# Performance work log

Measured on AMD Instinct MI355X. Metric: run time of the kernel, lower is better.

## Reference

```python
import jax, jax.numpy as jnp
import numpy as np

HEIGHT = 256
WIDTH = 256
SIGMAINV = 7000.0  # DIB-R style soft-silhouette sharpness
EPS = 1e-10


def setup_inputs():
    key = jax.random.key(0)
    k1, k2, k3, k4, k5 = jax.random.split(key, 5)
    B, P, F = 1, 160, 256
    TH = TW = 1024
    points_bxpx3 = 0.8 * jax.random.normal(k1, (B, P, 3), jnp.float32)
    faces_fx3 = jax.random.randint(k2, (F, 3), 0, P)
    camera_rot_bx3x3 = jnp.broadcast_to(jnp.eye(3, dtype=jnp.float32), (B, 3, 3))
    camera_pos_bx3 = jnp.tile(jnp.array([[0.0, 0.0, 2.5]], jnp.float32), (B, 1))
    camera_proj_3x1 = jnp.array([[2.5], [2.5], [-1.0]], jnp.float32)
    uv_bxpx2 = jax.random.uniform(k3, (B, P, 2), jnp.float32)
    ft_fx3 = jax.random.randint(k4, (F, 3), 0, P)
    texture_bx3xthxtw = jax.random.uniform(k5, (B, 3, TH, TW), jnp.float32)
    return {"points_bxpx3": points_bxpx3, "faces_fx3": faces_fx3,
            "camera_rot_bx3x3": camera_rot_bx3x3, "camera_pos_bx3": camera_pos_bx3,
            "camera_proj_3x1": camera_proj_3x1, "uv_bxpx2": uv_bxpx2,
            "ft_fx3": ft_fx3, "texture_bx3xthxtw": texture_bx3xthxtw}


def _perspective(points_bxpx3, faces_fx3, cam_rot, cam_pos, cam_proj):
    p = points_bxpx3 - cam_pos[:, None, :]
    p = jnp.einsum('bpj,bij->bpi', p, cam_rot)                  # camera frame [B,P,3]
    xy3 = p * cam_proj.reshape(1, 1, 3)
    xy = xy3[..., :2] / xy3[..., 2:3]                           # projected 2D [B,P,2]
    pf0 = p[:, faces_fx3[:, 0]]
    pf1 = p[:, faces_fx3[:, 1]]
    pf2 = p[:, faces_fx3[:, 2]]
    points3d_bxfx9 = jnp.concatenate([pf0, pf1, pf2], axis=2)
    points2d_bxfx6 = jnp.concatenate([xy[:, faces_fx3[:, 0]], xy[:, faces_fx3[:, 1]], xy[:, faces_fx3[:, 2]]], axis=2)
    normal_bxfx3 = jnp.cross(pf1 - pf0, pf2 - pf0)
    return points3d_bxfx9, points2d_bxfx6, normal_bxfx3


def _edge_dist2(px, py, ax, ay, bx, by):
    ex, ey = bx - ax, by - ay
    t = jnp.clip(((px - ax) * ex + (py - ay) * ey) / (ex * ex + ey * ey + EPS), 0.0, 1.0)
    dx, dy = px - (ax + t * ex), py - (ay + t * ey)
    return dx * dx + dy * dy


def _rasterize(points3d_bxfx9, points2d_bxfx6, normalz_bxfx1, feat_bxfx9, H, W):
    B, F, _ = points2d_bxfx6.shape
    x0, y0, x1, y1, x2, y2 = [points2d_bxfx6[:, None, :, i] for i in range(6)]   # [B,1,F]
    xs = (jnp.arange(W, dtype=jnp.float32) + 0.5) / W * 2.0 - 1.0
    ys = 1.0 - (jnp.arange(H, dtype=jnp.float32) + 0.5) / H * 2.0
    px = jnp.tile(xs[None, :], (H, 1)).reshape(1, -1, 1)                          # [1,N,1]
    py = jnp.tile(ys[:, None], (1, W)).reshape(1, -1, 1)
    A = (x1 - x0) * (y2 - y0) - (x2 - x0) * (y1 - y0)
    invA = jnp.where(jnp.abs(A) > EPS, 1.0 / jnp.where(jnp.abs(A) > EPS, A, 1.0), 0.0)
    w0 = ((x1 - px) * (y2 - py) - (x2 - px) * (y1 - py)) * invA                   # [B,N,F]
    w1 = ((x2 - px) * (y0 - py) - (x0 - px) * (y2 - py)) * invA
    w2 = 1.0 - w0 - w1
    valid = (jnp.abs(A) > EPS) & (normalz_bxfx1[:, None, :, 0] > 0)               # backface cull
    inside = (w0 >= 0) & (w1 >= 0) & (w2 >= 0) & valid
    z0 = points3d_bxfx9[:, None, :, 2]
    z1 = points3d_bxfx9[:, None, :, 5]
    z2 = points3d_bxfx9[:, None, :, 8]
    z = w0 * z0 + w1 * z1 + w2 * z2                                               # camera looks down -z
    fid = jnp.argmax(jnp.where(inside, z, -1e10), axis=2)                          # nearest covering face
    hit = jnp.any(inside, axis=2)
    take = lambda a: jnp.take_along_axis(a, fid[:, :, None], axis=2)[:, :, 0]
    w0s, w1s, w2s = take(w0), take(w1), take(w2)
    fverts = feat_bxfx9.reshape(B, F, 3, 3)
    fsel = jax.vmap(lambda fv, ii: fv[ii])(fverts, fid)                            # [B,N,3verts,3feat]
    imfeat = (w0s[..., None] * fsel[:, :, 0] + w1s[..., None] * fsel[:, :, 1] + w2s[..., None] * fsel[:, :, 2])
    imfeat = imfeat * hit[..., None].astype(imfeat.dtype)
    # soft silhouette probability (DIB-R): 1 - prod_f (1 - exp(-d^2 * sigmainv))
    d2 = jnp.minimum(_edge_dist2(px, py, x0, y0, x1, y1),
                     jnp.minimum(_edge_dist2(px, py, x1, y1, x2, y2),
                                 _edge_dist2(px, py, x2, y2, x0, y0)))
    d2 = jnp.where(inside, 0.0, d2)
    log_miss = jnp.log(jnp.clip(1.0 - jnp.exp(-d2 * SIGMAINV), 1e-10, 1.0))
    improb = 1.0 - jnp.exp(jnp.sum(jnp.where(valid, log_miss, 0.0), axis=2))
    return imfeat.reshape(B, H, W, 3), improb.reshape(B, H, W, 1)


def _fragmentshader(imtexcoord_bxhxwx2, texture_bx3xthxtw, hardmask_bxhxwx1):
    th, tw = texture_bx3xthxtw.shape[2], texture_bx3xthxtw.shape[3]
    x = imtexcoord_bxhxwx2[..., 0] * (tw - 1)
    y = (1.0 - imtexcoord_bxhxwx2[..., 1]) * (th - 1)
    x0f = jnp.clip(jnp.floor(x), 0, tw - 1)
    y0f = jnp.clip(jnp.floor(y), 0, th - 1)
    x0 = x0f.astype(jnp.int32)
    y0 = y0f.astype(jnp.int32)
    x1 = jnp.clip(x0 + 1, 0, tw - 1)
    y1 = jnp.clip(y0 + 1, 0, th - 1)
    wx = jnp.clip(x - x0f, 0.0, 1.0)[..., None]
    wy = jnp.clip(y - y0f, 0.0, 1.0)[..., None]
    tex = texture_bx3xthxtw.transpose(0, 2, 3, 1)                                 # [B,th,tw,3]
    g = jax.vmap(lambda t, yy, xx: t[yy, xx])
    c00, c01 = g(tex, y0, x0), g(tex, y0, x1)
    c10, c11 = g(tex, y1, x0), g(tex, y1, x1)
    color = (c00 * (1 - wx) + c01 * wx) * (1 - wy) + (c10 * (1 - wx) + c11 * wx) * wy
    return jnp.clip(color * hardmask_bxhxwx1, 0.0, 1.0)


def reference(points_bxpx3, faces_fx3, camera_rot_bx3x3, camera_pos_bx3, camera_proj_3x1, uv_bxpx2, ft_fx3, texture_bx3xthxtw):
    points3d, points2d, normal = _perspective(points_bxpx3, faces_fx3, camera_rot_bx3x3, camera_pos_bx3, camera_proj_3x1)
    normalz = normal[:, :, 2:3]
    normal1 = normal / (jnp.sqrt(jnp.sum(normal * normal, axis=2, keepdims=True)) + EPS)
    c0 = uv_bxpx2[:, ft_fx3[:, 0]]
    c1 = uv_bxpx2[:, ft_fx3[:, 1]]
    c2 = uv_bxpx2[:, ft_fx3[:, 2]]
    mask = jnp.ones_like(c0[:, :, :1])
    uv_bxfx9 = jnp.concatenate([c0, mask, c1, mask, c2, mask], axis=2)
    imfeat, improb = _rasterize(points3d, points2d, normalz, uv_bxfx9, HEIGHT, WIDTH)
    imrender = _fragmentshader(imfeat[..., :2], texture_bx3xthxtw, imfeat[..., 2:3])
    return imrender, improb, normal1
```

## Files before the change

kernel.cpp:

```cpp
#include <hip/hip_runtime.h>
#include <math.h>

#define HGT 256
#define WID 256
#define NF 256
#define NP 160
#define SIGMAINV 7000.0f
#define EPSF 1e-10f
#define TW 1024
#define TH 1024
#define CHUNKS 8
#define FPC 32
#define PPB 32
#define CUT2 3.29e-3f

struct FaceGeo {
    float x0, y0, x1, y1, x2, y2;
    float z0, z1, z2;
    float invA;
    float bminx, bminy, bmaxx, bmaxy;
    int   valid;
    int   pad;
};

__device__ __forceinline__ float mul_opaque(float a, float b)
{
    float r;
    asm volatile("v_mul_f32 %0, %1, %2" : "=v"(r) : "v"(a), "v"(b));
    return r;
}
__device__ __forceinline__ float fma_opaque(float a, float b, float c)
{
    float r;
    asm volatile("v_fma_f32 %0, %1, %2, %3" : "=v"(r) : "v"(a), "v"(b), "v"(c));
    return r;
}

__device__ __forceinline__ float edge_d2(float px, float py, float ax, float ay,
                                         float bx, float by)
{
    float ex = bx - ax, ey = by - ay;
    float t = ((px - ax) * ex + (py - ay) * ey) / (ex * ex + ey * ey + EPSF);
    t = fminf(fmaxf(t, 0.0f), 1.0f);
    float dx = px - (ax + t * ex);
    float dy = py - (ay + t * ey);
    return dx * dx + dy * dy;
}

__global__ __launch_bounds__(256) void render_fused(
    const float* __restrict__ pts,
    const int*   __restrict__ faces,
    const float* __restrict__ rot,
    const float* __restrict__ cpos,
    const float* __restrict__ proj,
    const float* __restrict__ uvs,
    const int*   __restrict__ ft,
    const float* __restrict__ tex,
    float*       __restrict__ out)
{
    __shared__ float4 sgeo4[NF * 4];
    __shared__ float  scratch[800];

    FaceGeo* sf  = (FaceGeo*)sgeo4;
    float*   sp  = scratch;
    float*   sxy = scratch + 480;
    float*   sZ   = scratch;
    float*   sLog = scratch + 256;
    int*     sFid = (int*)(scratch + 512);

    const int t = threadIdx.x;

    const float r00 = rot[0], r01 = rot[1], r02 = rot[2];
    const float r10 = rot[3], r11 = rot[4], r12 = rot[5];
    const float r20 = rot[6], r21 = rot[7], r22 = rot[8];
    const float cx = cpos[0], cy = cpos[1], cz = cpos[2];
    const float p0 = proj[0], p1 = proj[1], p2 = proj[2];

    if (t < NP) {
        float ax = pts[t * 3 + 0] - cx;
        float ay = pts[t * 3 + 1] - cy;
        float az = pts[t * 3 + 2] - cz;
        float qx = r00 * ax + r01 * ay + r02 * az;
        float qy = r10 * ax + r11 * ay + r12 * az;
        float qz = r20 * ax + r21 * ay + r22 * az;
        sp[t * 3 + 0] = qx; sp[t * 3 + 1] = qy; sp[t * 3 + 2] = qz;
        float zz = qz * p2;
        sxy[t * 2 + 0] = (qx * p0) / zz;
        sxy[t * 2 + 1] = (qy * p1) / zz;
    }
    __syncthreads();

    {
        int i0 = faces[t * 3 + 0], i1 = faces[t * 3 + 1], i2 = faces[t * 3 + 2];
        float ax = sp[i0 * 3 + 0], ay = sp[i0 * 3 + 1], az = sp[i0 * 3 + 2];
        float bx = sp[i1 * 3 + 0], by = sp[i1 * 3 + 1], bz = sp[i1 * 3 + 2];
        float gx = sp[i2 * 3 + 0], gy = sp[i2 * 3 + 1], gz = sp[i2 * 3 + 2];

        float e1x = bx - ax, e1y = by - ay, e1z = bz - az;
        float e2x = gx - ax, e2y = gy - ay, e2z = gz - az;
        float tnx = mul_opaque(e1z, e2y);
        float nx  = fma_opaque(e1y, e2z, -tnx);
        float tny = mul_opaque(e1x, e2z);
        float ny  = fma_opaque(e1z, e2x, -tny);
        float tnz = mul_opaque(e1y, e2x);
        float nz  = fma_opaque(e1x, e2y, -tnz);
        if (blockIdx.x == 0) {
            float s  = (mul_opaque(nx, nx) + mul_opaque(ny, ny)) + mul_opaque(nz, nz);
            float nl = sqrtf(s) + 1e-10f;
            float* out_normal = out + HGT * WID * 3 + HGT * WID;
            out_normal[t * 3 + 0] = nx / nl;
            out_normal[t * 3 + 1] = ny / nl;
            out_normal[t * 3 + 2] = nz / nl;
        }

        FaceGeo f;
        f.x0 = sxy[i0 * 2 + 0]; f.y0 = sxy[i0 * 2 + 1];
        f.x1 = sxy[i1 * 2 + 0]; f.y1 = sxy[i1 * 2 + 1];
        f.x2 = sxy[i2 * 2 + 0]; f.y2 = sxy[i2 * 2 + 1];
        f.z0 = az; f.z1 = bz; f.z2 = gz;
        float A = mul_opaque(f.x1 - f.x0, f.y2 - f.y0)
                - mul_opaque(f.x2 - f.x0, f.y1 - f.y0);
        bool okA = fabsf(A) > EPSF;
        f.invA  = okA ? 1.0f / A : 0.0f;
        f.valid = (okA && nz > 0.0f) ? 1 : 0;
        f.bminx = fminf(fminf(f.x0, f.x1), f.x2);
        f.bminy = fminf(fminf(f.y0, f.y1), f.y2);
        f.bmaxx = fmaxf(fmaxf(f.x0, f.x1), f.x2);
        f.bmaxy = fmaxf(fmaxf(f.y0, f.y1), f.y2);
        f.pad = 0;
        sf[t] = f;
    }
    __syncthreads();

    const int chunk = t >> 5;
    const int p     = t & 31;
    const int tx = (blockIdx.x & 31) * 8;
    const int ty = (blockIdx.x >> 5) * 4;
    {
        const int w = tx + (p & 7);
        const int h = ty + (p >> 3);
        const float px = ((float)w + 0.5f) / (float)WID * 2.0f - 1.0f;
        const float py = 1.0f - ((float)h + 0.5f) / (float)HGT * 2.0f;

        float best_z = -1e30f;
        int   fid = 0;
        float logsum = 0.0f;

        const int f0 = chunk * FPC;
        for (int f = f0; f < f0 + FPC; ++f) {
            const FaceGeo& fc = sf[f];
            if (!fc.valid) continue;
            float ddx = fmaxf(fmaxf(fc.bminx - px, px - fc.bmaxx), 0.0f);
            float ddy = fmaxf(fmaxf(fc.bminy - py, py - fc.bmaxy), 0.0f);
            if (ddx * ddx + ddy * ddy > CUT2) continue;

            float ax = fc.x1 - px, ay = fc.y1 - py;
            float bx = fc.x2 - px, by = fc.y2 - py;
            float gx = fc.x0 - px, gy = fc.y0 - py;
            float w0 = (ax * by - bx * ay) * fc.invA;
            float w1 = (bx * gy - gx * by) * fc.invA;
            float w2 = 1.0f - w0 - w1;
            bool inside = (w0 >= 0.0f) & (w1 >= 0.0f) & (w2 >= 0.0f);
            if (inside) {
                float z = w0 * fc.z0 + w1 * fc.z1 + w2 * fc.z2;
                if (z > best_z) { best_z = z; fid = f; }
                logsum += -23.025850929940457f;
            } else {
                float d2 = edge_d2(px, py, fc.x0, fc.y0, fc.x1, fc.y1);
                d2 = fminf(d2, edge_d2(px, py, fc.x1, fc.y1, fc.x2, fc.y2));
                d2 = fminf(d2, edge_d2(px, py, fc.x2, fc.y2, fc.x0, fc.y0));
                float a = d2 * SIGMAINV;
                if (a < 23.03f) {
                    float e = __expf(-a);
                    logsum += __logf(fmaxf(1.0f - e, 1e-10f));
                }
            }
        }
        sZ[t] = best_z; sFid[t] = fid; sLog[t] = logsum;
    }
    __syncthreads();

    if (t < PPB) {
        float bz = -1e30f; int bf = 0; float ls = 0.0f;
        #pragma unroll
        for (int c = 0; c < CHUNKS; ++c) {
            int i = c * PPB + t;
            ls += sLog[i];
            float z = sZ[i];
            if (z > bz) { bz = z; bf = sFid[i]; }
        }
        bool hit = bz > -1e29f;

        const int w = tx + (t & 7);
        const int h = ty + (t >> 3);
        const int pix = h * WID + w;
        out[HGT * WID * 3 + pix] = 1.0f - __expf(ls);

        float cr = 0.0f, cg = 0.0f, cb = 0.0f;
        if (hit) {
            const float px = ((float)w + 0.5f) / (float)WID * 2.0f - 1.0f;
            const float py = 1.0f - ((float)h + 0.5f) / (float)HGT * 2.0f;
            const FaceGeo& fc = sf[bf];
            float axx = fc.x1 - px, ayy = fc.y1 - py;
            float bxx = fc.x2 - px, byy = fc.y2 - py;
            float gxx = fc.x0 - px, gyy = fc.y0 - py;
            float w0 = (axx * byy - bxx * ayy) * fc.invA;
            float w1 = (bxx * gyy - gxx * byy) * fc.invA;
            float w2 = 1.0f - w0 - w1;
            int j0 = ft[bf * 3 + 0], j1 = ft[bf * 3 + 1], j2 = ft[bf * 3 + 2];
            float u = w0 * uvs[j0 * 2 + 0] + w1 * uvs[j1 * 2 + 0] + w2 * uvs[j2 * 2 + 0];
            float v = w0 * uvs[j0 * 2 + 1] + w1 * uvs[j1 * 2 + 1] + w2 * uvs[j2 * 2 + 1];
            float mask = w0 + w1 + w2;

            float x = u * (float)(TW - 1);
            float y = (1.0f - v) * (float)(TH - 1);
            float x0f = fminf(fmaxf(floorf(x), 0.0f), (float)(TW - 1));
            float y0f = fminf(fmaxf(floorf(y), 0.0f), (float)(TH - 1));
            int xi0 = (int)x0f, yi0 = (int)y0f;
            int xi1 = min(xi0 + 1, TW - 1);
            int yi1 = min(yi0 + 1, TH - 1);
            float wx = fminf(fmaxf(x - x0f, 0.0f), 1.0f);
            float wy = fminf(fmaxf(y - y0f, 0.0f), 1.0f);

            int o00 = yi0 * TW + xi0, o01 = yi0 * TW + xi1;
            int o10 = yi1 * TW + xi0, o11 = yi1 * TW + xi1;
            #pragma unroll
            for (int c = 0; c < 3; ++c) {
                const float* tp = tex + c * (TW * TH);
                float c00 = tp[o00], c01 = tp[o01], c10 = tp[o10], c11 = tp[o11];
                float col = (c00 * (1.0f - wx) + c01 * wx) * (1.0f - wy)
                          + (c10 * (1.0f - wx) + c11 * wx) * wy;
                col = fminf(fmaxf(col * mask, 0.0f), 1.0f);
                if (c == 0) cr = col; else if (c == 1) cg = col; else cb = col;
            }
        }
        out[pix * 3 + 0] = cr;
        out[pix * 3 + 1] = cg;
        out[pix * 3 + 2] = cb;
    }
}

extern "C" void kernel_launch(void* const* d_in, const int* in_sizes, int n_in,
                              void* d_out, int out_size, void* d_ws, size_t ws_size,
                              hipStream_t stream)
{
    const float* pts   = (const float*)d_in[0];
    const int*   faces = (const int*)  d_in[1];
    const float* rot   = (const float*)d_in[2];
    const float* cpos  = (const float*)d_in[3];
    const float* proj  = (const float*)d_in[4];
    const float* uvs   = (const float*)d_in[5];
    const int*   ft    = (const int*)  d_in[6];
    const float* tex   = (const float*)d_in[7];
    float* out = (float*)d_out;

    render_fused<<<(HGT * WID) / PPB, 256, 0, stream>>>(
        pts, faces, rot, cpos, proj, uvs, ft, tex, out);
}
```

Baseline: 98.56 us.

## Double pixels per block and pack face geometry into float4 records

Each block now covers an 8x8 pixel tile with 512 threads instead of 4x8 with 256. This halves the number of blocks that redundantly compute vertex projection and face setup. Face data is stored as four float4 records, and invalid faces get an impossible bounding box, so the inner loop does one vector load for the culling test and fetches the rest only when needed. Larger blocks may reduce occupancy and load-balancing flexibility.

```diff
diff --git a/kernel.cpp b/kernel.cpp
--- a/kernel.cpp
+++ b/kernel.cpp
@@ -11,17 +11,9 @@
 #define TH 1024
 #define CHUNKS 8
 #define FPC 32
-#define PPB 32
+#define PPB 64
+#define NTHR 512
 #define CUT2 3.29e-3f
-
-struct FaceGeo {
-    float x0, y0, x1, y1, x2, y2;
-    float z0, z1, z2;
-    float invA;
-    float bminx, bminy, bmaxx, bmaxy;
-    int   valid;
-    int   pad;
-};
 
 __device__ __forceinline__ float mul_opaque(float a, float b)
 {
@@ -47,7 +39,7 @@
     return dx * dx + dy * dy;
 }
 
-__global__ __launch_bounds__(256) void render_fused(
+__global__ __launch_bounds__(NTHR) void render_fused(
     const float* __restrict__ pts,
     const int*   __restrict__ faces,
     const float* __restrict__ rot,
@@ -59,14 +51,13 @@
     float*       __restrict__ out)
 {
     __shared__ float4 sgeo4[NF * 4];
-    __shared__ float  scratch[800];
-
-    FaceGeo* sf  = (FaceGeo*)sgeo4;
-    float*   sp  = scratch;
-    float*   sxy = scratch + 480;
-    float*   sZ   = scratch;
-    float*   sLog = scratch + 256;
-    int*     sFid = (int*)(scratch + 512);
+    __shared__ float  scratch[NTHR * 3];
+
+    float* sp  = scratch;
+    float* sxy = scratch + 480;
+    float* sZ   = scratch;
+    float* sLog = scratch + NTHR;
+    int*   sFid = (int*)(scratch + 2 * NTHR);
 
     const int t = threadIdx.x;
 
@@ -90,7 +81,7 @@
     }
     __syncthreads();
 
-    {
+    if (t < NF) {
         int i0 = faces[t * 3 + 0], i1 = faces[t * 3 + 1], i2 = faces[t * 3 + 2];
         float ax = sp[i0 * 3 + 0], ay = sp[i0 * 3 + 1], az = sp[i0 * 3 + 2];
         float bx = sp[i1 * 3 + 0], by = sp[i1 * 3 + 1], bz = sp[i1 * 3 + 2];
@@ -113,29 +104,34 @@
             out_normal[t * 3 + 2] = nz / nl;
         }
 
-        FaceGeo f;
-        f.x0 = sxy[i0 * 2 + 0]; f.y0 = sxy[i0 * 2 + 1];
-        f.x1 = sxy[i1 * 2 + 0]; f.y1 = sxy[i1 * 2 + 1];
-        f.x2 = sxy[i2 * 2 + 0]; f.y2 = sxy[i2 * 2 + 1];
-        f.z0 = az; f.z1 = bz; f.z2 = gz;
-        float A = mul_opaque(f.x1 - f.x0, f.y2 - f.y0)
-                - mul_opaque(f.x2 - f.x0, f.y1 - f.y0);
+        float x0 = sxy[i0 * 2 + 0], y0 = sxy[i0 * 2 + 1];
+        float x1 = sxy[i1 * 2 + 0], y1 = sxy[i1 * 2 + 1];
+        float x2 = sxy[i2 * 2 + 0], y2 = sxy[i2 * 2 + 1];
+        float A = mul_opaque(x1 - x0, y2 - y0) - mul_opaque(x2 - x0, y1 - y0);
         bool okA = fabsf(A) > EPSF;
-        f.invA  = okA ? 1.0f / A : 0.0f;
-        f.valid = (okA && nz > 0.0f) ? 1 : 0;
-        f.bminx = fminf(fminf(f.x0, f.x1), f.x2);
-        f.bminy = fminf(fminf(f.y0, f.y1), f.y2);
-        f.bmaxx = fmaxf(fmaxf(f.x0, f.x1), f.x2);
-        f.bmaxy = fmaxf(fmaxf(f.y0, f.y1), f.y2);
-        f.pad = 0;
-        sf[t] = f;
+        bool valid = okA && (nz > 0.0f);
+        float invA = okA ? 1.0f / A : 0.0f;
+
+        float4 q0;
+        if (valid) {
+            q0.x = fminf(fminf(x0, x1), x2);
+            q0.y = fminf(fminf(y0, y1), y2);
+            q0.z = fmaxf(fmaxf(x0, x1), x2);
+            q0.w = fmaxf(fmaxf(y0, y1), y2);
+        } else {
+            q0.x = 1e30f; q0.y = 1e30f; q0.z = -1e30f; q0.w = -1e30f;
+        }
+        sgeo4[t * 4 + 0] = q0;
+        sgeo4[t * 4 + 1] = make_float4(x0, y0, x1, y1);
+        sgeo4[t * 4 + 2] = make_float4(x2, y2, invA, az);
+        sgeo4[t * 4 + 3] = make_float4(bz, gz, 0.0f, 0.0f);
     }
     __syncthreads();
 
-    const int chunk = t >> 5;
-    const int p     = t & 31;
+    const int chunk = t >> 6;
+    const int p     = t & 63;
     const int tx = (blockIdx.x & 31) * 8;
-    const int ty = (blockIdx.x >> 5) * 4;
+    const int ty = (blockIdx.x >> 5) * 8;
     {
         const int w = tx + (p & 7);
         const int h = ty + (p >> 3);
@@ -148,27 +144,30 @@
 
         const int f0 = chunk * FPC;
         for (int f = f0; f < f0 + FPC; ++f) {
-            const FaceGeo& fc = sf[f];
-            if (!fc.valid) continue;
-            float ddx = fmaxf(fmaxf(fc.bminx - px, px - fc.bmaxx), 0.0f);
-            float ddy = fmaxf(fmaxf(fc.bminy - py, py - fc.bmaxy), 0.0f);
+            float4 q0 = sgeo4[f * 4 + 0];
+            float ddx = fmaxf(fmaxf(q0.x - px, px - q0.z), 0.0f);
+            float ddy = fmaxf(fmaxf(q0.y - py, py - q0.w), 0.0f);
             if (ddx * ddx + ddy * ddy > CUT2) continue;
 
-            float ax = fc.x1 - px, ay = fc.y1 - py;
-            float bx = fc.x2 - px, by = fc.y2 - py;
-            float gx = fc.x0 - px, gy = fc.y0 - py;
-            float w0 = (ax * by - bx * ay) * fc.invA;
-            float w1 = (bx * gy - gx * by) * fc.invA;
+            float4 q1 = sgeo4[f * 4 + 1];
+            float4 q2 = sgeo4[f * 4 + 2];
+
+            float ax = q1.z - px, ay = q1.w - py;
+            float bx = q2.x - px, by = q2.y - py;
+            float gx = q1.x - px, gy = q1.y - py;
+            float w0 = (ax * by - bx * ay) * q2.z;
+            float w1 = (bx * gy - gx * by) * q2.z;
             float w2 = 1.0f - w0 - w1;
             bool inside = (w0 >= 0.0f) & (w1 >= 0.0f) & (w2 >= 0.0f);
             if (inside) {
-                float z = w0 * fc.z0 + w1 * fc.z1 + w2 * fc.z2;
+                float4 q3 = sgeo4[f * 4 + 3];
+                float z = w0 * q2.w + w1 * q3.x + w2 * q3.y;
                 if (z > best_z) { best_z = z; fid = f; }
                 logsum += -23.025850929940457f;
             } else {
-                float d2 = edge_d2(px, py, fc.x0, fc.y0, fc.x1, fc.y1);
-                d2 = fminf(d2, edge_d2(px, py, fc.x1, fc.y1, fc.x2, fc.y2));
-                d2 = fminf(d2, edge_d2(px, py, fc.x2, fc.y2, fc.x0, fc.y0));
+                float d2 = edge_d2(px, py, q1.x, q1.y, q1.z, q1.w);
+                d2 = fminf(d2, edge_d2(px, py, q1.z, q1.w, q2.x, q2.y));
+                d2 = fminf(d2, edge_d2(px, py, q2.x, q2.y, q1.x, q1.y));
                 float a = d2 * SIGMAINV;
                 if (a < 23.03f) {
                     float e = __expf(-a);
@@ -200,12 +199,13 @@
         if (hit) {
             const float px = ((float)w + 0.5f) / (float)WID * 2.0f - 1.0f;
             const float py = 1.0f - ((float)h + 0.5f) / (float)HGT * 2.0f;
-            const FaceGeo& fc = sf[bf];
-            float axx = fc.x1 - px, ayy = fc.y1 - py;
-            float bxx = fc.x2 - px, byy = fc.y2 - py;
-            float gxx = fc.x0 - px, gyy = fc.y0 - py;
-            float w0 = (axx * byy - bxx * ayy) * fc.invA;
-            float w1 = (bxx * gyy - gxx * byy) * fc.invA;
+            float4 q1 = sgeo4[bf * 4 + 1];
+            float4 q2 = sgeo4[bf * 4 + 2];
+            float axx = q1.z - px, ayy = q1.w - py;
+            float bxx = q2.x - px, byy = q2.y - py;
+            float gxx = q1.x - px, gyy = q1.y - py;
+            float w0 = (axx * byy - bxx * ayy) * q2.z;
+            float w1 = (bxx * gyy - gxx * byy) * q2.z;
             float w2 = 1.0f - w0 - w1;
             int j0 = ft[bf * 3 + 0], j1 = ft[bf * 3 + 1], j2 = ft[bf * 3 + 2];
             float u = w0 * uvs[j0 * 2 + 0] + w1 * uvs[j1 * 2 + 0] + w2 * uvs[j2 * 2 + 0];
@@ -254,6 +254,6 @@
     const float* tex   = (const float*)d_in[7];
     float* out = (float*)d_out;
 
-    render_fused<<<(HGT * WID) / PPB, 256, 0, stream>>>(
+    render_fused<<<(HGT * WID) / PPB, NTHR, 0, stream>>>(
         pts, faces, rot, cpos, proj, uvs, ft, tex, out);
 }
```

Result: faster. 93.35 us (-5.3%).
